# Performance work log

Hardware: AMD Instinct MI355X
Metric: run time of the kernel (lower is better)

The kernel has to match this reference:

```python
import jax, jax.numpy as jnp
import numpy as np

D_MODEL, D_STATE, D_CONV, EXPAND, DT_RANK = 1024, 16, 4, 2, 64
D_INNER = EXPAND * D_MODEL


def setup_inputs() -> dict:
    key = jax.random.key(0)
    ks = jax.random.split(key, 10)
    B, L = 2, 2048
    x = jax.random.normal(ks[0], (B, L, D_MODEL), dtype=jnp.float32)
    # torch nn.Linear weights are [out, in]; applied as x @ W.T
    in_proj_w = jax.random.normal(ks[1], (2 * D_INNER, D_MODEL), jnp.float32) * (D_MODEL ** -0.5)
    conv_w = jax.random.normal(ks[2], (D_INNER, 1, D_CONV), jnp.float32) * (D_CONV ** -0.5)
    conv_b = jax.random.normal(ks[3], (D_INNER,), jnp.float32) * 0.01
    x_proj_w = jax.random.normal(ks[4], (DT_RANK + 2 * D_STATE, D_INNER), jnp.float32) * (D_INNER ** -0.5)
    dt_init_std = DT_RANK ** -0.5
    dt_proj_w = jax.random.uniform(ks[5], (D_INNER, DT_RANK), jnp.float32, -dt_init_std, dt_init_std)
    # dt bias init: inverse-softplus of dt ~ LogUniform(1e-3, 1e-1)
    dt = jnp.exp(jax.random.uniform(ks[6], (D_INNER,), jnp.float32) * (np.log(0.1) - np.log(0.001)) + np.log(0.001))
    dt_proj_b = dt + jnp.log(-jnp.expm1(-dt))
    A_log = jnp.log(jnp.tile(jnp.arange(1, D_STATE + 1, dtype=jnp.float32), (D_INNER, 1)))  # [D_INNER, N]
    D_skip = jnp.ones((D_INNER,), jnp.float32)
    out_proj_w = jax.random.normal(ks[7], (D_MODEL, D_INNER), jnp.float32) * (D_INNER ** -0.5)
    return {"x": x, "in_proj_w": in_proj_w, "conv_w": conv_w, "conv_b": conv_b,
            "x_proj_w": x_proj_w, "dt_proj_w": dt_proj_w, "dt_proj_b": dt_proj_b,
            "A_log": A_log, "D_skip": D_skip, "out_proj_w": out_proj_w}


def selective_scan(u, delta, A, Bmat, Cmat, D_skip):
    # u, delta: [B, L, D]; A: [D, N]; Bmat, Cmat: [B, L, N]; D_skip: [D]
    def step(h, inp):
        delta_t, B_t, C_t, u_t = inp  # [B,D], [B,N], [B,N], [B,D]
        dA = jnp.exp(delta_t[..., None] * A)                      # [B,D,N]
        h = dA * h + (delta_t * u_t)[..., None] * B_t[:, None, :]  # [B,D,N]
        y_t = jnp.einsum('bdn,bn->bd', h, C_t)
        return h, y_t
    B_size, L, D_size = u.shape
    h0 = jnp.zeros((B_size, D_size, A.shape[-1]), u.dtype)
    xs = (jnp.swapaxes(delta, 0, 1), jnp.swapaxes(Bmat, 0, 1),
          jnp.swapaxes(Cmat, 0, 1), jnp.swapaxes(u, 0, 1))
    _, ys = jax.lax.scan(step, h0, xs)          # ys: [L, B, D]
    y = jnp.swapaxes(ys, 0, 1)                  # [B, L, D]
    return y + u * D_skip


def reference(x, in_proj_w, conv_w, conv_b, x_proj_w, dt_proj_w, dt_proj_b, A_log, D_skip, out_proj_w):
    B_size, L, _ = x.shape
    xz = x @ in_proj_w.T                         # [B, L, 2*D_INNER]
    x_ssm, z = jnp.split(xz, 2, axis=-1)
    # causal depthwise conv1d (torch pads d_conv-1 both sides then takes [:L])
    x_c = jnp.swapaxes(x_ssm, 1, 2)              # [B, D_INNER, L]
    x_c = jax.lax.conv_general_dilated(
        x_c, conv_w, window_strides=(1,), padding=[(D_CONV - 1, 0)],
        dimension_numbers=('NCH', 'OIH', 'NCH'), feature_group_count=D_INNER)
    x_c = x_c + conv_b[None, :, None]
    x_ssm = jax.nn.silu(jnp.swapaxes(x_c, 1, 2))  # [B, L, D_INNER]
    x_dbl = x_ssm @ x_proj_w.T                    # [B, L, dt_rank + 2N]
    dt, Bm, Cm = jnp.split(x_dbl, [DT_RANK, DT_RANK + D_STATE], axis=-1)
    delta = jax.nn.softplus(dt @ dt_proj_w.T + dt_proj_b)  # [B, L, D_INNER]
    A = -jnp.exp(A_log)                           # [D_INNER, N]
    y = selective_scan(x_ssm, delta, A, Bm, Cm, D_skip)
    y = y * jax.nn.silu(z)
    return y @ out_proj_w.T                       # [B, L, d_model]
```

## Files before the change

### kernel.cpp

```cpp
#include <hip/hip_runtime.h>
#include <hip/hip_bf16.h>
#include <math.h>

#define NB      2
#define LSEQ    2048
#define BLTOK   4096
#define DM      1024
#define DI      2048
#define NST     16
#define DTR     64
#define CH      64
#define LC      32
#define LOG2E   1.44269504f

typedef __attribute__((ext_vector_type(8))) short short8;
typedef __attribute__((ext_vector_type(4))) float f32x4;

#define LDS_PTR(p) ((__attribute__((address_space(3))) void*)(p))
#define GLB_PTR(p) ((const __attribute__((address_space(1))) void*)(p))

static __device__ __forceinline__ unsigned short f2bf(float f) {
    unsigned int u = __float_as_uint(f);
    unsigned int r = (u + 0x7FFFu + ((u >> 16) & 1u)) >> 16;
    return (unsigned short)r;
}
static __device__ __forceinline__ float bf2f(unsigned short v) {
    return __uint_as_float((unsigned int)v << 16);
}

static __device__ __forceinline__ void pow_tree(float w, float* e) {
    e[0]  = w;
    e[1]  = e[0] * e[0];
    e[2]  = e[1] * e[0];
    e[3]  = e[1] * e[1];
    e[4]  = e[3] * e[0];
    e[5]  = e[3] * e[1];
    e[6]  = e[3] * e[2];
    e[7]  = e[3] * e[3];
    e[8]  = e[7] * e[0];
    e[9]  = e[7] * e[1];
    e[10] = e[7] * e[2];
    e[11] = e[7] * e[3];
    e[12] = e[7] * e[4];
    e[13] = e[7] * e[5];
    e[14] = e[7] * e[6];
    e[15] = e[7] * e[7];
}

#define C4_X   (BLTOK * DM / 4)
#define C4_W1  (2 * DI * DM / 4)
#define C4_W3  (96 * DI / 4)
#define C4_W6  (DM * DI / 4)
#define C4_W5  (DI * DTR / 4)
#define C4_TOT (C4_X + C4_W1 + C4_W3 + C4_W6 + C4_W5)

__launch_bounds__(256)
__global__ void cast_all(const float* __restrict__ x,   unsigned short* __restrict__ xb,
                         const float* __restrict__ w1,  unsigned short* __restrict__ wb1,
                         const float* __restrict__ w3,  unsigned short* __restrict__ wb3,
                         const float* __restrict__ w6,  unsigned short* __restrict__ wb6,
                         const float* __restrict__ w5,  unsigned short* __restrict__ wb5)
{
    int i = blockIdx.x * 256 + threadIdx.x;
    if (i >= C4_TOT) return;
    const float* in; unsigned short* out;
    if (i < C4_X)                         { in = x;  out = xb;  }
    else if ((i -= C4_X) < C4_W1)         { in = w1; out = wb1; }
    else if ((i -= C4_W1) < C4_W3)        { in = w3; out = wb3; }
    else if ((i -= C4_W3) < C4_W6)        { in = w6; out = wb6; }
    else       { i -= C4_W6;                in = w5; out = wb5; }
    float4 v = ((const float4*)in)[i];
    uint2 o;
    o.x = (unsigned)f2bf(v.x) | ((unsigned)f2bf(v.y) << 16);
    o.y = (unsigned)f2bf(v.z) | ((unsigned)f2bf(v.w) << 16);
    ((uint2*)out)[i] = o;
}

template<int EPI>
__launch_bounds__(256)
__global__ void gemm_db(const unsigned short* __restrict__ A,
                        const unsigned short* __restrict__ W,
                        void* __restrict__ Cout,
                        const float* __restrict__ bias,
                        int M, int N, int K, int lda, int ldb, int ldc)
{
    __shared__ unsigned short lds[2][2][128 * 64];

    const int tid = threadIdx.x;
    const int l = tid & 63;
    const int w = tid >> 6;
    const int wr = w >> 1, wc = w & 1;
    const int brow = blockIdx.y * 128;
    const int bcol = blockIdx.x * 128;

    const int strow = tid >> 3;
    const int scol  = ((tid & 7) ^ (strow & 7)) * 8;

    f32x4 acc[4][4];
#pragma unroll
    for (int i = 0; i < 4; ++i)
#pragma unroll
        for (int j = 0; j < 4; ++j) acc[i][j] = (f32x4)0.f;

    auto stage = [&](int bb, int k0) {
#pragma unroll
        for (int i = 0; i < 4; ++i) {
            const unsigned short* ga = A + (size_t)(brow + i * 32 + strow) * lda + k0 + scol;
            __builtin_amdgcn_global_load_lds(GLB_PTR(ga),
                LDS_PTR((char*)&lds[bb][0][0] + (i * 32 + w * 8) * 128), 16, 0, 0);
            const unsigned short* gb = W + (size_t)(bcol + i * 32 + strow) * ldb + k0 + scol;
            __builtin_amdgcn_global_load_lds(GLB_PTR(gb),
                LDS_PTR((char*)&lds[bb][1][0] + (i * 32 + w * 8) * 128), 16, 0, 0);
        }
    };

    auto compute = [&](int bb) {
        const char* baseA = (const char*)&lds[bb][0][0];
        const char* baseB = (const char*)&lds[bb][1][0];
        const int xo  = (l & 7) * 16;
        const int ko0 = (l >> 4) * 16;
#pragma unroll
        for (int ks = 0; ks < 2; ++ks) {
            const int kb = ks * 64 + ko0;
            short8 af[4], bfr[4];
#pragma unroll
            for (int i = 0; i < 4; ++i) {
                const int rowA = wr * 64 + i * 16 + (l & 15);
                af[i] = *(const short8*)(baseA + rowA * 128 + (kb ^ xo));
                const int rowB = wc * 64 + i * 16 + (l & 15);
                bfr[i] = *(const short8*)(baseB + rowB * 128 + (kb ^ xo));
            }
#pragma unroll
            for (int i = 0; i < 4; ++i)
#pragma unroll
                for (int j = 0; j < 4; ++j)
                    acc[i][j] = __builtin_amdgcn_mfma_f32_16x16x32_bf16(af[i], bfr[j], acc[i][j], 0, 0, 0);
        }
    };

    const int nt = K / 64;
    stage(0, 0);
    __syncthreads();
    int cur = 0;
    for (int t = 0; t < nt - 1; ++t) {
        stage(cur ^ 1, (t + 1) * 64);
        compute(cur);
        __syncthreads();
        cur ^= 1;
    }
    compute(cur);

#pragma unroll
    for (int i = 0; i < 4; ++i) {
        const int row0 = brow + wr * 64 + i * 16 + ((l >> 4) * 4);
#pragma unroll
        for (int j = 0; j < 4; ++j) {
            const int col = bcol + wc * 64 + j * 16 + (l & 15);
            if (EPI == 1) {
                unsigned short* Cb = (unsigned short*)Cout;
#pragma unroll
                for (int r = 0; r < 4; ++r)
                    Cb[(size_t)(row0 + r) * ldc + col] = f2bf(acc[i][j][r]);
            } else if (EPI == 3) {
                const float bv = bias[col];
#pragma unroll
                for (int r = 0; r < 4; ++r) {
                    float v = acc[i][j][r] + bv;
                    v = (v > 20.f) ? v : log1pf(__expf(v));
                    ((unsigned short*)Cout)[(size_t)(row0 + r) * ldc + col] = f2bf(v);
                }
            } else {
                float* Cf = (float*)Cout;
#pragma unroll
                for (int r = 0; r < 4; ++r)
                    Cf[(size_t)(row0 + r) * ldc + col] = acc[i][j][r];
            }
        }
    }
}

__launch_bounds__(256)
__global__ void gemm_mfma_sk(const unsigned short* __restrict__ A,
                             const unsigned short* __restrict__ W,
                             float* __restrict__ Cpart,
                             int M, int N, int K, int lda, int ldb, int ldc, int kslices)
{
    __shared__ unsigned short Asub[128 * 32];
    __shared__ unsigned short Bsub[128 * 32];

    const int tid = threadIdx.x;
    const int l = tid & 63;
    const int w = tid >> 6;
    const int wr = w >> 1, wc = w & 1;
    const int brow = blockIdx.y * 128;
    const int bcol = blockIdx.x * 128;
    const int ks = blockIdx.z;
    const int klen = K / kslices;
    const int kbeg = ks * klen;
    float* C = Cpart + (size_t)ks * M * ldc;

    f32x4 acc[4][4];
#pragma unroll
    for (int i = 0; i < 4; ++i)
#pragma unroll
        for (int j = 0; j < 4; ++j) acc[i][j] = (f32x4)0.f;

    const int srow = tid >> 2;
    const int scol = (tid & 3) * 8;

    for (int k0 = kbeg; k0 < kbeg + klen; k0 += 32) {
#pragma unroll
        for (int i = 0; i < 2; ++i) {
            const int ar = brow + i * 64 + srow;
            const unsigned short* ga = A + (size_t)ar * lda + k0 + scol;
            __builtin_amdgcn_global_load_lds(GLB_PTR(ga),
                LDS_PTR((char*)Asub + i * 4096 + w * 1024), 16, 0, 0);
            int nr = bcol + i * 64 + srow;
            if (nr > N - 1) nr = N - 1;
            const unsigned short* gb = W + (size_t)nr * ldb + k0 + scol;
            __builtin_amdgcn_global_load_lds(GLB_PTR(gb),
                LDS_PTR((char*)Bsub + i * 4096 + w * 1024), 16, 0, 0);
        }
        __syncthreads();

        short8 af[4], bf[4];
#pragma unroll
        for (int i = 0; i < 4; ++i) {
            const int row = wr * 64 + i * 16 + (l & 15);
            af[i] = *(const short8*)((const char*)Asub + row * 64 + (l >> 4) * 16);
        }
#pragma unroll
        for (int j = 0; j < 4; ++j) {
            const int row = wc * 64 + j * 16 + (l & 15);
            bf[j] = *(const short8*)((const char*)Bsub + row * 64 + (l >> 4) * 16);
        }
#pragma unroll
        for (int i = 0; i < 4; ++i)
#pragma unroll
            for (int j = 0; j < 4; ++j)
                acc[i][j] = __builtin_amdgcn_mfma_f32_16x16x32_bf16(af[i], bf[j], acc[i][j], 0, 0, 0);
        __syncthreads();
    }

#pragma unroll
    for (int i = 0; i < 4; ++i) {
        const int row0 = brow + wr * 64 + i * 16 + ((l >> 4) * 4);
#pragma unroll
        for (int j = 0; j < 4; ++j) {
            const int col = bcol + wc * 64 + j * 16 + (l & 15);
            if (col < N) {
#pragma unroll
                for (int r = 0; r < 4; ++r)
                    C[(size_t)(row0 + r) * ldc + col] = acc[i][j][r];
            }
        }
    }
}

__launch_bounds__(256)
__global__ void sk_reduce(const float* __restrict__ part, float* __restrict__ out,
                          unsigned short* __restrict__ dtb, int n4, int slices)
{
    int i = blockIdx.x * 256 + threadIdx.x;
    if (i < n4) {
        float4 s = ((const float4*)part)[i];
        for (int k = 1; k < slices; ++k) {
            float4 p = ((const float4*)part)[(size_t)k * n4 + i];
            s.x += p.x; s.y += p.y; s.z += p.z; s.w += p.w;
        }
        ((float4*)out)[i] = s;
        const int r = i / 24, cq = i % 24;
        if (cq < 16) {
            uint2 o;
            o.x = (unsigned)f2bf(s.x) | ((unsigned)f2bf(s.y) << 16);
            o.y = (unsigned)f2bf(s.z) | ((unsigned)f2bf(s.w) << 16);
            *(uint2*)&dtb[(size_t)r * DTR + cq * 4] = o;
        }
    }
}

__launch_bounds__(256)
__global__ void conv_silu_kernel(const unsigned short* __restrict__ xzb,
                                 const float* __restrict__ cw,
                                 const float* __restrict__ cb,
                                 unsigned short* __restrict__ ub)
{
    const int orig = blockIdx.x;
    const int bl = (orig & 7) * (BLTOK / 8) + (orig >> 3);
    const int l  = bl & (LSEQ - 1);
    const int d0 = threadIdx.x * 8;

    float acc[8];
    float4 w4[8];
#pragma unroll
    for (int q = 0; q < 8; ++q) {
        w4[q]  = *(const float4*)&cw[(d0 + q) * 4];
        acc[q] = cb[d0 + q];
    }
#pragma unroll
    for (int k = 0; k < 4; ++k) {
        const int ls = l - 3 + k;
        if (ls < 0) continue;
        short8 v = *(const short8*)&xzb[(size_t)(bl - 3 + k) * (2 * DI) + d0];
#pragma unroll
        for (int q = 0; q < 8; ++q) {
            const float wk = ((const float*)&w4[q])[k];
            acc[q] = fmaf(wk, bf2f((unsigned short)v[q]), acc[q]);
        }
    }
    short8 o;
#pragma unroll
    for (int q = 0; q < 8; ++q) {
        const float s = acc[q] / (1.f + __expf(-acc[q]));
        o[q] = (short)f2bf(s);
    }
    *(short8*)&ub[(size_t)bl * DI + d0] = o;
}

__launch_bounds__(256)
__global__ void scan_phase1(const unsigned short* __restrict__ delta,
                            const unsigned short* __restrict__ ub,
                            const float* __restrict__ xdbl, const float* __restrict__ A_log,
                            unsigned short* __restrict__ S, float* __restrict__ dsum_out)
{
    __shared__ float sB[LC][NST];
    const int tid = threadIdx.x;
    const int d = blockIdx.x * 256 + tid;
    const int c = blockIdx.y;
    const int b = blockIdx.z;
    const int t0 = c * LC;

    for (int i = tid; i < LC * NST; i += 256)
        sB[i >> 4][i & 15] = xdbl[(size_t)(b * LSEQ + t0 + (i >> 4)) * 96 + 64 + (i & 15)];
    __syncthreads();

    const float Av0 = -__expf(A_log[d * NST]) * LOG2E;
    bool fast = true;
    for (int n = 1; n < NST; ++n) {
        const float avn = -__expf(A_log[d * NST + n]) * LOG2E;
        fast &= (fabsf(avn - (float)(n + 1) * Av0) <= 1e-3f * fabsf(avn));
    }

    float Sv[NST];
    float dsum = 0.f;
#pragma unroll
    for (int n = 0; n < NST; ++n) Sv[n] = 0.f;

    const unsigned short* dbase = delta + (size_t)(b * LSEQ + t0) * DI + d;
    const unsigned short* ubase = ub    + (size_t)(b * LSEQ + t0) * DI + d;

    if (fast) {
        for (int tg = 0; tg < LC; tg += 4) {
            float dl[4], uu[4];
#pragma unroll
            for (int q = 0; q < 4; ++q) {
                dl[q] = bf2f(dbase[(size_t)(tg + q) * DI]);
                uu[q] = bf2f(ubase[(size_t)(tg + q) * DI]);
            }
#pragma unroll
            for (int q = 0; q < 4; ++q) {
                const float du = dl[q] * uu[q];
                dsum += dl[q];
                float e[NST];
                pow_tree(__builtin_amdgcn_exp2f(dl[q] * Av0), e);
#pragma unroll
                for (int n = 0; n < NST; ++n)
                    Sv[n] = fmaf(e[n], Sv[n], du * sB[tg + q][n]);
            }
        }
    } else {
        for (int t = 0; t < LC; ++t) {
            const float dlt = bf2f(dbase[(size_t)t * DI]);
            const float uu  = bf2f(ubase[(size_t)t * DI]);
            const float du  = dlt * uu;
            dsum += dlt;
            for (int n = 0; n < NST; ++n) {
                const float avn = -__expf(A_log[d * NST + n]) * LOG2E;
                const float dA = __builtin_amdgcn_exp2f(dlt * avn);
                Sv[n] = fmaf(dA, Sv[n], du * sB[t][n]);
            }
        }
    }

    const size_t base = ((size_t)(b * CH + c) * DI + d) * NST;
    short8 s0, s1;
#pragma unroll
    for (int n = 0; n < 8; ++n) { s0[n] = (short)f2bf(Sv[n]); s1[n] = (short)f2bf(Sv[8 + n]); }
    *(short8*)&S[base]     = s0;
    *(short8*)&S[base + 8] = s1;
    dsum_out[(size_t)(b * CH + c) * DI + d] = dsum;
}

__launch_bounds__(256)
__global__ void scan_phase2(const unsigned short* __restrict__ S, const float* __restrict__ dsum,
                            const float* __restrict__ A_log, unsigned short* __restrict__ hin)
{
    const int g = blockIdx.x * 256 + threadIdx.x;
    const int n = g & 15;
    const int d = (g >> 4) & (DI - 1);
    const int b = g >> 15;
    const float avn = -__expf(A_log[d * NST + n]) * LOG2E;
    float h = 0.f;
    for (int c = 0; c < CH; ++c) {
        const size_t idx = ((size_t)(b * CH + c) * DI + d) * NST + n;
        hin[idx] = f2bf(h);
        const float Pc = __builtin_amdgcn_exp2f(dsum[(size_t)(b * CH + c) * DI + d] * avn);
        h = fmaf(Pc, h, bf2f(S[idx]));
    }
}

__launch_bounds__(256)
__global__ void scan_phase3(const unsigned short* __restrict__ delta,
                            const unsigned short* __restrict__ ub,
                            const float* __restrict__ xdbl, const float* __restrict__ A_log,
                            const float* __restrict__ Dskip, const unsigned short* __restrict__ xzb,
                            const unsigned short* __restrict__ hin, unsigned short* __restrict__ yg)
{
    __shared__ float sB[LC][NST], sC[LC][NST];
    const int tid = threadIdx.x;
    const int d = blockIdx.x * 256 + tid;
    const int c = blockIdx.y;
    const int b = blockIdx.z;
    const int t0 = c * LC;

    for (int i = tid; i < LC * NST; i += 256) {
        const size_t row = (size_t)(b * LSEQ + t0 + (i >> 4)) * 96;
        sB[i >> 4][i & 15] = xdbl[row + 64 + (i & 15)];
        sC[i >> 4][i & 15] = xdbl[row + 80 + (i & 15)];
    }
    __syncthreads();

    const float Av0 = -__expf(A_log[d * NST]) * LOG2E;
    bool fast = true;
    for (int n = 1; n < NST; ++n) {
        const float avn = -__expf(A_log[d * NST + n]) * LOG2E;
        fast &= (fabsf(avn - (float)(n + 1) * Av0) <= 1e-3f * fabsf(avn));
    }

    float h[NST];
    const size_t hbase = ((size_t)(b * CH + c) * DI + d) * NST;
    {
        short8 h0 = *(const short8*)&hin[hbase];
        short8 h1 = *(const short8*)&hin[hbase + 8];
#pragma unroll
        for (int n = 0; n < 8; ++n) {
            h[n]     = bf2f((unsigned short)h0[n]);
            h[8 + n] = bf2f((unsigned short)h1[n]);
        }
    }
    const float Dskv = Dskip[d];

    const unsigned short* dbase = delta + (size_t)(b * LSEQ + t0) * DI + d;
    const unsigned short* ubase = ub    + (size_t)(b * LSEQ + t0) * DI + d;
    const unsigned short* zbase = xzb   + (size_t)(b * LSEQ + t0) * (2 * DI) + DI + d;
    unsigned short* yrow = yg + (size_t)(b * LSEQ + t0) * DI + d;

    if (fast) {
        for (int tg = 0; tg < LC; tg += 4) {
            float dl[4], uu[4], zz[4];
#pragma unroll
            for (int q = 0; q < 4; ++q) {
                dl[q] = bf2f(dbase[(size_t)(tg + q) * DI]);
                uu[q] = bf2f(ubase[(size_t)(tg + q) * DI]);
                zz[q] = bf2f(zbase[(size_t)(tg + q) * (2 * DI)]);
            }
#pragma unroll
            for (int q = 0; q < 4; ++q) {
                const float du = dl[q] * uu[q];
                float e[NST];
                pow_tree(__builtin_amdgcn_exp2f(dl[q] * Av0), e);
                float y = 0.f;
#pragma unroll
                for (int n = 0; n < NST; ++n) {
                    h[n] = fmaf(e[n], h[n], du * sB[tg + q][n]);
                    y = fmaf(h[n], sC[tg + q][n], y);
                }
                const float zv = zz[q];
                const float sig = __frcp_rn(1.f + __expf(-zv));
                const float val = (y + uu[q] * Dskv) * (zv * sig);
                yrow[(size_t)(tg + q) * DI] = f2bf(val);
            }
        }
    } else {
        for (int t = 0; t < LC; ++t) {
            const float dlt = bf2f(dbase[(size_t)t * DI]);
            const float uu  = bf2f(ubase[(size_t)t * DI]);
            const float zv  = bf2f(zbase[(size_t)t * (2 * DI)]);
            const float du  = dlt * uu;
            float y = 0.f;
            for (int n = 0; n < NST; ++n) {
                const float avn = -__expf(A_log[d * NST + n]) * LOG2E;
                const float dA = __builtin_amdgcn_exp2f(dlt * avn);
                h[n] = fmaf(dA, h[n], du * sB[t][n]);
                y = fmaf(h[n], sC[t][n], y);
            }
            const float sig = __frcp_rn(1.f + __expf(-zv));
            const float val = (y + uu * Dskv) * (zv * sig);
            yrow[(size_t)t * DI] = f2bf(val);
        }
    }
}

extern "C" void kernel_launch(void* const* d_in, const int* in_sizes, int n_in,
                              void* d_out, int out_size, void* d_ws, size_t ws_size,
                              hipStream_t stream)
{
    const float* x        = (const float*)d_in[0];
    const float* in_w     = (const float*)d_in[1];
    const float* conv_w   = (const float*)d_in[2];
    const float* conv_b   = (const float*)d_in[3];
    const float* xproj_w  = (const float*)d_in[4];
    const float* dtproj_w = (const float*)d_in[5];
    const float* dtproj_b = (const float*)d_in[6];
    const float* A_log    = (const float*)d_in[7];
    const float* Dskip    = (const float*)d_in[8];
    const float* out_w    = (const float*)d_in[9];
    float* out = (float*)d_out;

    char* ws = (char*)d_ws;
#define MB(x) ((size_t)(x) * 1024 * 1024)
    unsigned short* xzb   = (unsigned short*)(ws);
    unsigned short* ub    = (unsigned short*)(ws + MB(32));
    unsigned short* delta = (unsigned short*)(ws + MB(48));
    float*          xdbl  = (float*)(ws + MB(64));
    unsigned short* ygb   = (unsigned short*)(ws + MB(66));
    unsigned short* S     = (unsigned short*)(ws + MB(82));
    float*          dsum  = (float*)(ws + MB(90));
    unsigned short* hin   = (unsigned short*)(ws + MB(91));
    unsigned short* xb    = (unsigned short*)(ws + MB(99));
    unsigned short* wb1   = (unsigned short*)(ws + MB(107));
    unsigned short* wb3   = (unsigned short*)(ws + MB(115));
    unsigned short* wb6   = (unsigned short*)(ws + MB(116));
    unsigned short* wb5   = (unsigned short*)(ws + MB(120));
    unsigned short* dtb   = (unsigned short*)(ws + MB(121));
    float*          xdbl_part = (float*)(ws + MB(122));

    dim3 blk(256);

    cast_all<<<dim3((C4_TOT + 255) / 256), blk, 0, stream>>>(x, xb, in_w, wb1, xproj_w, wb3,
                                                             out_w, wb6, dtproj_w, wb5);

    gemm_db<1><<<dim3(32, 32), blk, 0, stream>>>(xb, wb1, xzb, nullptr,
                                                 BLTOK, 2 * DI, DM, DM, DM, 2 * DI);

    conv_silu_kernel<<<dim3(BLTOK), blk, 0, stream>>>(xzb, conv_w, conv_b, ub);

    gemm_mfma_sk<<<dim3(1, 32, 8), blk, 0, stream>>>(ub, wb3, xdbl_part,
                                                     BLTOK, DTR + 2 * NST, DI, DI, DI, 96, 8);
    sk_reduce<<<dim3((BLTOK * 96 / 4 + 255) / 256), blk, 0, stream>>>(xdbl_part, xdbl, dtb,
                                                                      BLTOK * 96 / 4, 8);

    gemm_db<3><<<dim3(16, 32), blk, 0, stream>>>(dtb, wb5, delta, dtproj_b,
                                                 BLTOK, DI, DTR, DTR, DTR, DI);

    scan_phase1<<<dim3(DI / 256, CH, NB), blk, 0, stream>>>(delta, ub, xdbl, A_log, S, dsum);
    scan_phase2<<<dim3(NB * DI * NST / 256), blk, 0, stream>>>(S, dsum, A_log, hin);
    scan_phase3<<<dim3(DI / 256, CH, NB), blk, 0, stream>>>(delta, ub, xdbl, A_log, Dskip,
                                                            xzb, hin, ygb);

    gemm_db<0><<<dim3(8, 32), blk, 0, stream>>>(ygb, wb6, out, nullptr,
                                                BLTOK, DM, DI, DI, DI, DM);
}
```

Measured before the change: 216.3 us.

## Use 256x256-tile 8-wave GEMM with quarter-phase prefetch for in_proj

Result: no change. 219.6 us (+1.6%).

```diff
diff --git a/kernel.cpp b/kernel.cpp
--- a/kernel.cpp
+++ b/kernel.cpp
@@ -76,6 +76,116 @@
     ((uint2*)out)[i] = o;
 }
 
+__launch_bounds__(512, 2)
+__global__ void gemm_8ph(const unsigned short* __restrict__ A,
+                         const unsigned short* __restrict__ W,
+                         unsigned short* __restrict__ Cout,
+                         int M, int N, int K, int lda, int ldb, int ldc)
+{
+    __shared__ unsigned short lds[2][2][256 * 64];
+
+    const int tid = threadIdx.x;
+    const int l   = tid & 63;
+    const int wid = tid >> 6;
+    const int wr  = wid >> 2;
+    const int wc  = wid & 3;
+    const int brow = blockIdx.y * 256;
+    const int bcol = blockIdx.x * 256;
+
+    const int strow = tid >> 3;
+    const int sslot = tid & 7;
+
+    f32x4 acc[8][4];
+#pragma unroll
+    for (int i = 0; i < 8; ++i)
+#pragma unroll
+        for (int j = 0; j < 4; ++j) acc[i][j] = (f32x4)0.f;
+
+    auto stage_q = [&](int bb, int q, int k0) {
+        const int ab   = q >> 1;
+        const int half = q & 1;
+        const unsigned short* src = ab ? W : A;
+        const int ld    = ab ? ldb : lda;
+        const int rbase = (ab ? bcol : brow) + half * 128;
+#pragma unroll
+        for (int i = 0; i < 2; ++i) {
+            const int r   = i * 64 + strow;
+            const int col = (sslot ^ (r & 7)) * 8;
+            const unsigned short* g = src + (size_t)(rbase + r) * ld + k0 + col;
+            __builtin_amdgcn_global_load_lds(GLB_PTR(g),
+                LDS_PTR((char*)&lds[bb][ab][0] + half * 16384 + i * 8192 + wid * 1024),
+                16, 0, 0);
+        }
+    };
+
+    const int xo  = (l & 7) * 16;
+    const int ko0 = (l >> 4) * 16;
+
+    const int NT = K / 64;
+#pragma unroll
+    for (int q = 0; q < 4; ++q) stage_q(0, q, 0);
+    __syncthreads();
+
+    for (int kt = 0; kt < NT; ++kt) {
+        const int p = kt & 1;
+        const bool pf = (kt + 1 < NT);
+        const int k1 = (kt + 1) * 64;
+        const char* baseA = (const char*)&lds[p][0][0];
+        const char* baseB = (const char*)&lds[p][1][0];
+#pragma unroll
+        for (int q = 0; q < 4; ++q) {
+            const int mh = q >> 1, nh = q & 1;
+            if (pf) stage_q(p ^ 1, q, k1);
+            short8 af[2][4], bfr[2][2];
+#pragma unroll
+            for (int ks = 0; ks < 2; ++ks) {
+                const int kb = ks * 64 + ko0;
+#pragma unroll
+                for (int i = 0; i < 4; ++i) {
+                    const int rowA = wr * 128 + mh * 64 + i * 16 + (l & 15);
+                    af[ks][i] = *(const short8*)(baseA + (size_t)rowA * 128 + (kb ^ xo));
+                }
+#pragma unroll
+                for (int j = 0; j < 2; ++j) {
+                    const int rowB = wc * 64 + nh * 32 + j * 16 + (l & 15);
+                    bfr[ks][j] = *(const short8*)(baseB + (size_t)rowB * 128 + (kb ^ xo));
+                }
+            }
+            __builtin_amdgcn_sched_barrier(0);
+            __builtin_amdgcn_s_barrier();
+            __builtin_amdgcn_sched_barrier(0);
+            __builtin_amdgcn_s_setprio(1);
+#pragma unroll
+            for (int ks = 0; ks < 2; ++ks)
+#pragma unroll
+                for (int i = 0; i < 4; ++i)
+#pragma unroll
+                    for (int j = 0; j < 2; ++j)
+                        acc[mh * 4 + i][nh * 2 + j] = __builtin_amdgcn_mfma_f32_16x16x32_bf16(
+                            af[ks][i], bfr[ks][j], acc[mh * 4 + i][nh * 2 + j], 0, 0, 0);
+            __builtin_amdgcn_s_setprio(0);
+            if (q < 3) {
+                __builtin_amdgcn_sched_barrier(0);
+                __builtin_amdgcn_s_barrier();
+                __builtin_amdgcn_sched_barrier(0);
+            }
+        }
+        __syncthreads();
+    }
+
+#pragma unroll
+    for (int mi = 0; mi < 8; ++mi) {
+        const int row0 = brow + wr * 128 + mi * 16 + ((l >> 4) * 4);
+#pragma unroll
+        for (int nj = 0; nj < 4; ++nj) {
+            const int col = bcol + wc * 64 + nj * 16 + (l & 15);
+#pragma unroll
+            for (int r = 0; r < 4; ++r)
+                Cout[(size_t)(row0 + r) * ldc + col] = f2bf(acc[mi][nj][r]);
+        }
+    }
+}
+
 template<int EPI>
 __launch_bounds__(256)
 __global__ void gemm_db(const unsigned short* __restrict__ A,
@@ -540,8 +650,8 @@
     cast_all<<<dim3((C4_TOT + 255) / 256), blk, 0, stream>>>(x, xb, in_w, wb1, xproj_w, wb3,
                                                              out_w, wb6, dtproj_w, wb5);
 
-    gemm_db<1><<<dim3(32, 32), blk, 0, stream>>>(xb, wb1, xzb, nullptr,
-                                                 BLTOK, 2 * DI, DM, DM, DM, 2 * DI);
+    gemm_8ph<<<dim3(16, 16), dim3(512), 0, stream>>>(xb, wb1, xzb,
+                                                     BLTOK, 2 * DI, DM, DM, DM, 2 * DI);
 
     conv_silu_kernel<<<dim3(BLTOK), blk, 0, stream>>>(xzb, conv_w, conv_b, ub);
 
```

## Add 4-stage K=32 pipelined GEMM for in_proj and out_proj

Applied to the files above, without the earlier changes.

Result: no change. 220.1 us (+1.8%).

```diff
diff --git a/kernel.cpp b/kernel.cpp
--- a/kernel.cpp
+++ b/kernel.cpp
@@ -78,6 +78,109 @@
 
 template<int EPI>
 __launch_bounds__(256)
+__global__ void gemm_ks(const unsigned short* __restrict__ A,
+                        const unsigned short* __restrict__ W,
+                        void* __restrict__ Cout,
+                        int M, int N, int K, int lda, int ldb, int ldc)
+{
+    __shared__ unsigned short lds[4][2][128 * 32];
+
+    const int tid = threadIdx.x;
+    const int l = tid & 63;
+    const int w = tid >> 6;
+    const int wr = w >> 1, wc = w & 1;
+    const int brow = blockIdx.y * 128;
+    const int bcol = blockIdx.x * 128;
+
+    f32x4 acc[4][4];
+#pragma unroll
+    for (int i = 0; i < 4; ++i)
+#pragma unroll
+        for (int j = 0; j < 4; ++j) acc[i][j] = (f32x4)0.f;
+
+    const int strow0 = tid >> 2;
+    auto stage = [&](int s) {
+        const int slot = s & 3;
+        const int k0 = s * 32;
+#pragma unroll
+        for (int i = 0; i < 2; ++i) {
+            const int r = i * 64 + strow0;
+            const int f = (r & 3) ^ ((r >> 2) & 3);
+            const int col = ((tid & 3) ^ f) * 8;
+            const unsigned short* ga = A + (size_t)(brow + r) * lda + k0 + col;
+            __builtin_amdgcn_global_load_lds(GLB_PTR(ga),
+                LDS_PTR((char*)&lds[slot][0][0] + (i * 64 + w * 16) * 64), 16, 0, 0);
+            const unsigned short* gb = W + (size_t)(bcol + r) * ldb + k0 + col;
+            __builtin_amdgcn_global_load_lds(GLB_PTR(gb),
+                LDS_PTR((char*)&lds[slot][1][0] + (i * 64 + w * 16) * 64), 16, 0, 0);
+        }
+    };
+
+    const int fl = (l & 3) ^ ((l >> 2) & 3);
+    const int g  = l >> 4;
+    const int ro = ((g ^ fl) << 4);
+
+    auto compute = [&](int s) {
+        const int slot = s & 3;
+        const char* baseA = (const char*)&lds[slot][0][0];
+        const char* baseB = (const char*)&lds[slot][1][0];
+        short8 af[4], bfr[4];
+#pragma unroll
+        for (int i = 0; i < 4; ++i) {
+            const int rA = wr * 64 + i * 16 + (l & 15);
+            af[i] = *(const short8*)(baseA + rA * 64 + ro);
+            const int rB = wc * 64 + i * 16 + (l & 15);
+            bfr[i] = *(const short8*)(baseB + rB * 64 + ro);
+        }
+#pragma unroll
+        for (int i = 0; i < 4; ++i)
+#pragma unroll
+            for (int j = 0; j < 4; ++j)
+                acc[i][j] = __builtin_amdgcn_mfma_f32_16x16x32_bf16(af[i], bfr[j], acc[i][j], 0, 0, 0);
+    };
+
+    const int NS = K / 32;
+    stage(0); stage(1); stage(2);
+
+    for (int s = 0; s < NS - 2; ++s) {
+        asm volatile("s_waitcnt vmcnt(8)" ::: "memory");
+        __builtin_amdgcn_s_barrier();
+        __builtin_amdgcn_sched_barrier(0);
+        if (s + 3 < NS) stage(s + 3);
+        compute(s);
+    }
+    asm volatile("s_waitcnt vmcnt(4)" ::: "memory");
+    __builtin_amdgcn_s_barrier();
+    __builtin_amdgcn_sched_barrier(0);
+    compute(NS - 2);
+    asm volatile("s_waitcnt vmcnt(0)" ::: "memory");
+    __builtin_amdgcn_s_barrier();
+    __builtin_amdgcn_sched_barrier(0);
+    compute(NS - 1);
+
+#pragma unroll
+    for (int i = 0; i < 4; ++i) {
+        const int row0 = brow + wr * 64 + i * 16 + ((l >> 4) * 4);
+#pragma unroll
+        for (int j = 0; j < 4; ++j) {
+            const int col = bcol + wc * 64 + j * 16 + (l & 15);
+            if (EPI == 1) {
+                unsigned short* Cb = (unsigned short*)Cout;
+#pragma unroll
+                for (int r = 0; r < 4; ++r)
+                    Cb[(size_t)(row0 + r) * ldc + col] = f2bf(acc[i][j][r]);
+            } else {
+                float* Cf = (float*)Cout;
+#pragma unroll
+                for (int r = 0; r < 4; ++r)
+                    Cf[(size_t)(row0 + r) * ldc + col] = acc[i][j][r];
+            }
+        }
+    }
+}
+
+template<int EPI>
+__launch_bounds__(256)
 __global__ void gemm_db(const unsigned short* __restrict__ A,
                         const unsigned short* __restrict__ W,
                         void* __restrict__ Cout,
@@ -540,7 +643,7 @@
     cast_all<<<dim3((C4_TOT + 255) / 256), blk, 0, stream>>>(x, xb, in_w, wb1, xproj_w, wb3,
                                                              out_w, wb6, dtproj_w, wb5);
 
-    gemm_db<1><<<dim3(32, 32), blk, 0, stream>>>(xb, wb1, xzb, nullptr,
+    gemm_ks<1><<<dim3(32, 32), blk, 0, stream>>>(xb, wb1, xzb,
                                                  BLTOK, 2 * DI, DM, DM, DM, 2 * DI);
 
     conv_silu_kernel<<<dim3(BLTOK), blk, 0, stream>>>(xzb, conv_w, conv_b, ub);
@@ -558,6 +661,6 @@
     scan_phase3<<<dim3(DI / 256, CH, NB), blk, 0, stream>>>(delta, ub, xdbl, A_log, Dskip,
                                                             xzb, hin, ygb);
 
-    gemm_db<0><<<dim3(8, 32), blk, 0, stream>>>(ygb, wb6, out, nullptr,
+    gemm_ks<0><<<dim3(8, 32), blk, 0, stream>>>(ygb, wb6, out,
                                                 BLTOK, DM, DI, DI, DI, DM);
 }
```
